# Optimization experiments

Measured on AMD Instinct MI355X. Metric: run time of the kernel, lower is better.

## Reference

```python
import jax, jax.numpy as jnp
import numpy as np

NJ, NS, NM, NR = 100000, 20000, 10000, 5000
D_IN, OUT, H = 128, 256, 4
C = OUT // H
E = 250000
NEG_SLOPE = 0.2
LN_EPS = 1e-5


def setup_inputs() -> dict:
    key = jax.random.key(0)
    ks = jax.random.split(key, 24)
    inp = {
        'x_job':     jax.random.normal(ks[0], (NJ, D_IN), jnp.float32),
        'x_station': jax.random.normal(ks[1], (NS, D_IN), jnp.float32),
        'x_machine': jax.random.normal(ks[2], (NM, D_IN), jnp.float32),
        'x_robot':   jax.random.normal(ks[3], (NR, D_IN), jnp.float32),
        'src_cl': jax.random.randint(ks[4],  (E,), 0, NS, jnp.int32),
        'dst_cl': jax.random.randint(ks[5],  (E,), 0, NJ, jnp.int32),
        'src_ld': jax.random.randint(ks[6],  (E,), 0, NS, jnp.int32),
        'dst_ld': jax.random.randint(ks[7],  (E,), 0, NJ, jnp.int32),
        'src_we': jax.random.randint(ks[8],  (E,), 0, NM, jnp.int32),
        'dst_we': jax.random.randint(ks[9],  (E,), 0, NJ, jnp.int32),
        'src_ex': jax.random.randint(ks[10], (E,), 0, NM, jnp.int32),
        'dst_ex': jax.random.randint(ks[11], (E,), 0, NJ, jnp.int32),
        'src_hd': jax.random.randint(ks[12], (E,), 0, NR, jnp.int32),
        'dst_hd': jax.random.randint(ks[13], (E,), 0, NJ, jnp.int32),
        'Ws':      jax.random.normal(ks[14], (5, D_IN, OUT), jnp.float32) * 0.05,
        'att_src': jax.random.normal(ks[15], (5, H, C), jnp.float32) * 0.05,
        'att_dst': jax.random.normal(ks[16], (5, H, C), jnp.float32) * 0.05,
        'biases':  jnp.zeros((5, OUT), jnp.float32),
        'W_res':   jax.random.normal(ks[17], (D_IN, OUT), jnp.float32) * 0.05,
        'ln_gamma': jnp.ones((OUT,), jnp.float32),
        'ln_beta':  jnp.zeros((OUT,), jnp.float32),
    }
    return inp


def _gat(x_src, x_dst, src, dst, W, a_src, a_dst, b):
    # Bipartite GATConv (PyG semantics, shared lin for src and dst, concat heads)
    hs = (x_src @ W).reshape(-1, H, C)   # [Ns,H,C]
    hd = (x_dst @ W).reshape(-1, H, C)   # [Nd,H,C]
    a_s = jnp.einsum('nhc,hc->nh', hs, a_src)  # [Ns,H]
    a_d = jnp.einsum('nhc,hc->nh', hd, a_dst)  # [Nd,H]
    e = jax.nn.leaky_relu(a_s[src] + a_d[dst], NEG_SLOPE)  # [E,H]
    # softmax over incoming edges of each dst node
    m = jax.ops.segment_max(e, dst, num_segments=NJ)       # [Nd,H]
    ex = jnp.exp(e - m[dst])
    denom = jax.ops.segment_sum(ex, dst, num_segments=NJ)
    alpha = ex / (denom[dst] + 1e-16)                       # [E,H]
    msg = alpha[:, :, None] * hs[src]                        # [E,H,C]
    out = jax.ops.segment_sum(msg, dst, num_segments=NJ)    # [Nd,H,C]
    return out.reshape(NJ, H * C) + b


def reference(x_job, x_station, x_machine, x_robot,
              src_cl, dst_cl, src_ld, dst_ld, src_we, dst_we,
              src_ex, dst_ex, src_hd, dst_hd,
              Ws, att_src, att_dst, biases, W_res, ln_gamma, ln_beta):
    rels = [
        (x_station, src_cl, dst_cl),
        (x_station, src_ld, dst_ld),
        (x_machine, src_we, dst_we),
        (x_machine, src_ex, dst_ex),
        (x_robot,   src_hd, dst_hd),
    ]
    acc = jnp.zeros((NJ, OUT), x_job.dtype)
    for i, (xs, s, d) in enumerate(rels):  # sum aggregation across relations
        acc = acc + _gat(xs, x_job, s, d, Ws[i], att_src[i], att_dst[i], biases[i])
    h = acc + x_job @ W_res                # residual projection (dj != out_dim)
    h = jax.nn.relu(h)
    mu = jnp.mean(h, axis=-1, keepdims=True)
    var = jnp.var(h, axis=-1, keepdims=True)
    return (h - mu) * jax.lax.rsqrt(var + LN_EPS) * ln_gamma + ln_beta
```

## Files before the change

### kernel.cpp

```cpp
#include <hip/hip_runtime.h>

typedef unsigned short u16;
typedef unsigned int u32;
typedef unsigned long long u64;
typedef __attribute__((ext_vector_type(8))) short s16x8;
typedef __attribute__((ext_vector_type(4))) float f32x4;

__device__ __forceinline__ float bf2f(u16 u) { return __uint_as_float(((u32)u) << 16); }
__device__ __forceinline__ u16 f2bf(float f) {
    u32 b = __float_as_uint(f);
    b += 0x7fffu + ((b >> 16) & 1u);
    return (u16)(b >> 16);
}

__global__ void probe_mark(float* __restrict__ out, int n, float val) {
    int i = blockIdx.x * blockDim.x + threadIdx.x;
    if (i < n) out[i] = val;
}

struct PrepX { const float* x[4]; int rows[4]; int blks[4]; u16* xb[4]; };

__global__ void k_prep_all(const float* __restrict__ Ws, const float* __restrict__ W_res,
                           const float* __restrict__ att_src, const float* __restrict__ att_dst,
                           const float* __restrict__ biases,
                           u32* __restrict__ cnt, int zc, int nzb, u16* __restrict__ wt,
                           float* __restrict__ w_d_all, float* __restrict__ w_s_cat,
                           float* __restrict__ bias_sum, PrepX PX) {
    int b = blockIdx.x;
    if (b < nzb) {
        int i = b * 256 + threadIdx.x;
        if (i < zc) cnt[i] = 0u;
        return;
    }
    b -= nzb;
    if (b < 768) {
        int i = b * 256 + threadIdx.x;
        int k = i & 127;
        int c = (i >> 7) & 255;
        int w = i >> 15;
        float v = (w < 5) ? Ws[(size_t)w * 32768 + k * 256 + c] : W_res[k * 256 + c];
        wt[i] = f2bf(v);
        return;
    }
    b -= 768;
    if (b < 6) {
        if (b < 5) {
            int k = threadIdx.x;
            if (k >= 128) return;
            const float* Wr = Ws + (size_t)b * 128 * 256 + (size_t)k * 256;
            for (int h = 0; h < 4; ++h) {
                float ss = 0.f, sd = 0.f;
                for (int c = 0; c < 64; ++c) {
                    float w = Wr[h * 64 + c];
                    ss += w * att_src[(b * 4 + h) * 64 + c];
                    sd += w * att_dst[(b * 4 + h) * 64 + c];
                }
                w_d_all[k * 20 + b * 4 + h] = sd;
                w_s_cat[b * 512 + k * 4 + h] = ss;
            }
        } else if (threadIdx.x < 256) {
            float s = 0.f;
            for (int r = 0; r < 5; ++r) s += biases[r * 256 + threadIdx.x];
            bias_sum[threadIdx.x] = s;
        }
        return;
    }
    b -= 6;
#pragma unroll
    for (int a = 0; a < 4; ++a) {
        if (b < PX.blks[a]) {
            int elem = b * 2048 + threadIdx.x * 8;
            if (elem < PX.rows[a] * 128) {
                const float4* src = (const float4*)(PX.x[a] + elem);
                float4 v0 = src[0], v1 = src[1];
                u32 w0 = ((u32)f2bf(v0.y) << 16) | f2bf(v0.x);
                u32 w1 = ((u32)f2bf(v0.w) << 16) | f2bf(v0.z);
                u32 w2 = ((u32)f2bf(v1.y) << 16) | f2bf(v1.x);
                u32 w3 = ((u32)f2bf(v1.w) << 16) | f2bf(v1.z);
                *(uint4*)(PX.xb[a] + elem) = make_uint4(w0, w1, w2, w3);
            }
            return;
        }
        b -= PX.blks[a];
    }
}

struct SDesc { const float* A; const float* W; float* out; int N; int Kout; int groups; int start; };
struct STab { SDesc d[6]; int total; };
struct GDesc { const u16* A; u16* C; int wslice; int N; int start; };
struct GTab { GDesc d[6]; };
struct EdgeP { const int* src[5]; const int* dst[5]; int base[5]; };

__global__ __launch_bounds__(256) void k_mid(GTab T, const u16* __restrict__ wt,
                                             STab S, EdgeP P,
                                             u32* __restrict__ cnt, u32* __restrict__ epos,
                                             int E, int nEB, int G, int C, int SB) {
    __shared__ __align__(16) u16 sA[64][136];
    __shared__ __align__(16) u16 sB[64][136];
    int q = blockIdx.x / 11, p = blockIdx.x % 11;
    int t = threadIdx.x;

    if (p < 3) {
        int bx = q * 3 + p;
        if (bx >= G) return;
        int mi = 0;
#pragma unroll
        for (int i = 1; i < 6; ++i) if (bx >= T.d[i].start) mi = i;
        GDesc d = T.d[mi];
        int R0 = (bx - d.start) * 64;
        int r = t >> 2, seg = (t & 3) * 32;
        {
            uint4 a0, a1, a2, a3;
            if (R0 + r < d.N) {
                const uint4* pa = (const uint4*)(d.A + (size_t)(R0 + r) * 128 + seg);
                a0 = pa[0]; a1 = pa[1]; a2 = pa[2]; a3 = pa[3];
            } else {
                a0 = a1 = a2 = a3 = make_uint4(0, 0, 0, 0);
            }
            uint4* qd = (uint4*)&sA[r][seg];
            qd[0] = a0; qd[1] = a1; qd[2] = a2; qd[3] = a3;
        }
        int wave = t >> 6, lane = t & 63;
        int quad = lane >> 4, m = lane & 15;
        const u16* aRow = &sA[wave * 16 + m][0];
        const u16* wbase = wt + (size_t)d.wslice * 32768;

        for (int y = 0; y < 4; ++y) {
            int c0 = y * 64;
            const uint4* pb = (const uint4*)(wbase + (size_t)(c0 + r) * 128 + seg);
            uint4 b0 = pb[0], b1 = pb[1], b2 = pb[2], b3 = pb[3];
            __syncthreads();
            uint4* qb = (uint4*)&sB[r][seg];
            qb[0] = b0; qb[1] = b1; qb[2] = b2; qb[3] = b3;
            __syncthreads();

            f32x4 acc[4] = {};
#pragma unroll
            for (int k0 = 0; k0 < 128; k0 += 32) {
                s16x8 af = *(const s16x8*)(aRow + k0 + quad * 8);
#pragma unroll
                for (int ct = 0; ct < 4; ++ct) {
                    s16x8 bf = *(const s16x8*)(&sB[ct * 16 + m][k0 + quad * 8]);
                    acc[ct] = __builtin_amdgcn_mfma_f32_16x16x32_bf16(af, bf, acc[ct], 0, 0, 0);
                }
            }
#pragma unroll
            for (int ct = 0; ct < 4; ++ct) {
#pragma unroll
                for (int i = 0; i < 4; ++i) {
                    int row = R0 + wave * 16 + quad * 4 + i;
                    if (row < d.N) d.C[(size_t)row * 256 + c0 + ct * 16 + m] = f2bf(acc[ct][i]);
                }
            }
        }
    } else if (p < 8) {
        int i = q * 5 + (p - 3);
        if (i >= C) return;
        int r = i / nEB, eb = i - r * nEB;
        int e = eb * 256 + t;
        if (e >= E) return;
        u32 c = atomicAdd(cnt + (size_t)P.dst[r][e] * 5 + r, 1u);
        epos[(size_t)r * E + e] = c;
    } else {
        int i = q * 3 + (p - 8);
        if (i >= SB) return;
        int idx = i * 256 + t;
        if (idx >= S.total) return;
        int mi = 0;
#pragma unroll
        for (int j = 1; j < 6; ++j) if (idx >= S.d[j].start) mi = j;
        SDesc d = S.d[mi];
        int local = idx - d.start;
        int row = local / d.groups, g = local - row * d.groups;
        const float* a = d.A + (size_t)row * 128;
        const float* w = d.W + g * 4;
        int Kout = d.Kout;
        float s0 = 0.f, s1 = 0.f, s2 = 0.f, s3 = 0.f;
        for (int k = 0; k < 128; k += 4) {
            float4 av = *(const float4*)(a + k);
            float4 w0 = *(const float4*)(w + (size_t)(k + 0) * Kout);
            float4 w1 = *(const float4*)(w + (size_t)(k + 1) * Kout);
            float4 w2 = *(const float4*)(w + (size_t)(k + 2) * Kout);
            float4 w3 = *(const float4*)(w + (size_t)(k + 3) * Kout);
            s0 += av.x * w0.x + av.y * w1.x + av.z * w2.x + av.w * w3.x;
            s1 += av.x * w0.y + av.y * w1.y + av.z * w2.y + av.w * w3.y;
            s2 += av.x * w0.z + av.y * w1.z + av.z * w2.z + av.w * w3.z;
            s3 += av.x * w0.w + av.y * w1.w + av.z * w2.w + av.w * w3.w;
        }
        float* o = d.out + (size_t)row * Kout + g * 4;
        *(float4*)o = make_float4(s0, s1, s2, s3);
    }
}

__global__ void k_scan1(const u32* __restrict__ cnt, u32* __restrict__ off,
                        u32* __restrict__ bsum, int nblk) {
    int b = blockIdx.x, t = threadIdx.x;
    size_t base = (size_t)b * 1024 + t * 4;
    u32 v0 = cnt[base], v1 = cnt[base + 1], v2 = cnt[base + 2], v3 = cnt[base + 3];
    u32 tsum = v0 + v1 + v2 + v3;
    __shared__ u32 s[256];
    u32 x = tsum;
    s[t] = x; __syncthreads();
    for (int ofs = 1; ofs < 256; ofs <<= 1) {
        u32 y = (t >= ofs) ? s[t - ofs] : 0u;
        __syncthreads();
        x += y; s[t] = x;
        __syncthreads();
    }
    u32 ex = x - tsum;
    off[base] = ex; off[base + 1] = ex + v0; off[base + 2] = ex + v0 + v1; off[base + 3] = ex + v0 + v1 + v2;
    if (t == 255) bsum[b] = x;
}

__global__ void k_scan23(u32* __restrict__ off, const u32* __restrict__ bsum, int nblk) {
    int b = blockIdx.x, t = threadIdx.x;
    __shared__ u32 s[256];
    u32 part = 0;
    for (int i = t; i < b; i += 256) part += bsum[i];
    s[t] = part; __syncthreads();
    for (int ofs = 128; ofs; ofs >>= 1) {
        if (t < ofs) s[t] += s[t + ofs];
        __syncthreads();
    }
    u32 add = s[0];
    size_t base = (size_t)b * 1024 + t * 4;
    off[base] += add; off[base + 1] += add; off[base + 2] += add; off[base + 3] += add;
}

__global__ void k_fill(EdgeP P, const u32* __restrict__ off, const u32* __restrict__ epos,
                       u32* __restrict__ epay, int E) {
    int r = blockIdx.y;
    int e = blockIdx.x * blockDim.x + threadIdx.x;
    if (e >= E) return;
    int d = P.dst[r][e];
    u32 pos = off[(size_t)d * 5 + r] + epos[(size_t)r * E + e];
    epay[pos] = (u32)(P.base[r] + P.src[r][e]);
}

__global__ __launch_bounds__(512) void k_gather(
        const u32* __restrict__ offs, const u32* __restrict__ epay,
        const float* __restrict__ as_h,
        const float* __restrict__ a_d,
        const u16* __restrict__ hs, const u16* __restrict__ resb,
        const float* __restrict__ bias_sum,
        const float* __restrict__ gamma, const float* __restrict__ beta,
        float* __restrict__ out, int NJ) {
    int row = blockIdx.x * 8 + (threadIdx.x >> 6);
    int lane = threadIdx.x & 63;
    if (row >= NJ) return;

    ushort4 rr = *(const ushort4*)(resb + (size_t)row * 256 + lane * 4);
    float4 bb = *(const float4*)(bias_sum + lane * 4);
    int c = lane * 4;
    float4 g = *(const float4*)(gamma + c);
    float4 be = *(const float4*)(beta + c);

    int hd = lane >> 4;
    u32 hoff = (u32)(lane << 2);

    const float* adb = a_d + (size_t)row * 20 + hd;
    float adx[5] = { adb[0], adb[4], adb[8], adb[12], adb[16] };

    const u32* op = offs + (size_t)row * 5;
    u32 o[6];
#pragma unroll
    for (int i = 0; i < 6; ++i) o[i] = op[i];
    u32 deg = o[5] - o[0];

    u32 pv = 0;
    if (deg) {
        u32 li = (u32)lane < deg ? (u32)lane : 0u;
        pv = epay[o[0] + li];
    }

    float a0 = 0.f, a1 = 0.f, a2 = 0.f, a3 = 0.f;
#pragma unroll
    for (int r = 0; r < 5; ++r) {
        float adr = adx[r];
        float n0 = 0.f, n1 = 0.f, n2 = 0.f, n3 = 0.f, dsum = 0.f;
        for (u32 e = o[r]; e < o[r + 1]; ++e) {
            u32 i = e - o[0];
            u32 p;
            if (i < 64u) p = __shfl(pv, (int)i);
            else         p = epay[e];
            float x = as_h[p * 4 + (u32)hd] + adr;
            x = x > 0.f ? x : 0.2f * x;
            float w = __expf(x);
            dsum += w;
            ushort4 hv = *(const ushort4*)(hs + ((size_t)p << 8) + hoff);
            n0 += w * bf2f(hv.x); n1 += w * bf2f(hv.y);
            n2 += w * bf2f(hv.z); n3 += w * bf2f(hv.w);
        }
        float iv = 1.f / (dsum + 1e-16f);
        a0 += n0 * iv; a1 += n1 * iv; a2 += n2 * iv; a3 += n3 * iv;
    }

    float h0 = fmaxf(a0 + bf2f(rr.x) + bb.x, 0.f);
    float h1 = fmaxf(a1 + bf2f(rr.y) + bb.y, 0.f);
    float h2 = fmaxf(a2 + bf2f(rr.z) + bb.z, 0.f);
    float h3 = fmaxf(a3 + bf2f(rr.w) + bb.w, 0.f);
    float s = h0 + h1 + h2 + h3;
    float s2 = h0 * h0 + h1 * h1 + h2 * h2 + h3 * h3;
    for (int o2 = 32; o2; o2 >>= 1) {
        s += __shfl_xor(s, o2);
        s2 += __shfl_xor(s2, o2);
    }
    float mu = s * (1.f / 256.f);
    float var = s2 * (1.f / 256.f) - mu * mu;
    float rs = rsqrtf(var + 1e-5f);
    float4 o4;
    o4.x = (h0 - mu) * rs * g.x + be.x;
    o4.y = (h1 - mu) * rs * g.y + be.y;
    o4.z = (h2 - mu) * rs * g.z + be.z;
    o4.w = (h3 - mu) * rs * g.w + be.w;
    *(float4*)(out + (size_t)row * 256 + c) = o4;
}

static size_t align256(size_t x) { return (x + 255) & ~(size_t)255; }

extern "C" void kernel_launch(void* const* d_in, const int* in_sizes, int n_in,
                              void* d_out, int out_size, void* d_ws, size_t ws_size,
                              hipStream_t stream) {
    float* out = (float*)d_out;

    int NJ = in_sizes[0] / 128, NS = in_sizes[1] / 128, NM = in_sizes[2] / 128, NR = in_sizes[3] / 128;
    int E = in_sizes[4];
    bool cfg_ok = (n_in >= 21) && (out_size == NJ * 256)
        && (in_sizes[14] == 5 * 128 * 256) && (in_sizes[18] == 128 * 256)
        && (in_sizes[19] == 256) && (in_sizes[20] == 256);
    if (!cfg_ok) { probe_mark<<<8, 256, 0, stream>>>(out, 2048, 1000000.0f); return; }

    const float* x_job = (const float*)d_in[0];
    const float* x_st  = (const float*)d_in[1];
    const float* x_ma  = (const float*)d_in[2];
    const float* x_ro  = (const float*)d_in[3];
    EdgeP EP;
    EP.src[0] = (const int*)d_in[4];  EP.dst[0] = (const int*)d_in[5];
    EP.src[1] = (const int*)d_in[6];  EP.dst[1] = (const int*)d_in[7];
    EP.src[2] = (const int*)d_in[8];  EP.dst[2] = (const int*)d_in[9];
    EP.src[3] = (const int*)d_in[10]; EP.dst[3] = (const int*)d_in[11];
    EP.src[4] = (const int*)d_in[12]; EP.dst[4] = (const int*)d_in[13];
    EP.base[0] = 0; EP.base[1] = NS; EP.base[2] = 2 * NS;
    EP.base[3] = 2 * NS + NM; EP.base[4] = 2 * NS + 2 * NM;
    const float* Ws      = (const float*)d_in[14];
    const float* att_src = (const float*)d_in[15];
    const float* att_dst = (const float*)d_in[16];
    const float* biases  = (const float*)d_in[17];
    const float* W_res   = (const float*)d_in[18];
    const float* gamma   = (const float*)d_in[19];
    const float* beta    = (const float*)d_in[20];

    int nseg = 5 * NJ;
    int nblk = (nseg + 1023) / 1024;
    int NPAD = nblk * 1024;
    int TOT = 2 * NS + 2 * NM + NR;
    int TOTX = NJ + NS + NM + NR;

    char* base = (char*)d_ws;
    size_t ob = 0;
    float*  w_d_all  = (float*)(base + ob);  ob += align256(128 * 20 * 4);
    float*  w_s_cat  = (float*)(base + ob);  ob += align256(5 * 128 * 4 * 4);
    float*  bias_sum = (float*)(base + ob);  ob += align256(256 * 4);
    float*  a_d      = (float*)(base + ob);  ob += align256((size_t)NJ * 20 * 4);
    float*  as_cat   = (float*)(base + ob);  ob += align256((size_t)TOT * 4 * 4);
    u16*    wt       = (u16*)(base + ob);    ob += align256((size_t)6 * 256 * 128 * 2);
    u16*    xb       = (u16*)(base + ob);    ob += align256((size_t)TOTX * 128 * 2);
    u16*    resb     = (u16*)(base + ob);    ob += align256((size_t)NJ * 256 * 2);
    u16*    hs_cat   = (u16*)(base + ob);    ob += align256((size_t)TOT * 256 * 2);
    u32*    cnt      = (u32*)(base + ob);    ob += align256((size_t)NPAD * 4);
    u32*    offs     = (u32*)(base + ob);    ob += align256((size_t)NPAD * 4);
    u32*    bsum     = (u32*)(base + ob);    ob += align256((size_t)nblk * 4);
    u32*    epos     = (u32*)(base + ob);    ob += align256((size_t)5 * E * 4);
    u32*    epay     = (u32*)(base + ob);    ob += align256((size_t)5 * E * 4);

    if (ws_size < ob) { probe_mark<<<8, 256, 0, stream>>>(out, 2048, 500000.0f); return; }

    int zc = NPAD;
    int nzb = (zc + 255) / 256;
    PrepX PX;
    PX.x[0] = x_job; PX.x[1] = x_st; PX.x[2] = x_ma; PX.x[3] = x_ro;
    PX.rows[0] = NJ; PX.rows[1] = NS; PX.rows[2] = NM; PX.rows[3] = NR;
    u16* xb_job = xb;
    u16* xb_st  = xb + (size_t)NJ * 128;
    u16* xb_ma  = xb + (size_t)(NJ + NS) * 128;
    u16* xb_ro  = xb + (size_t)(NJ + NS + NM) * 128;
    PX.xb[0] = xb_job; PX.xb[1] = xb_st; PX.xb[2] = xb_ma; PX.xb[3] = xb_ro;
    int nxb = 0;
    for (int a = 0; a < 4; ++a) { PX.blks[a] = (PX.rows[a] * 128 + 2047) / 2048; nxb += PX.blks[a]; }
    k_prep_all<<<nzb + 768 + 6 + nxb, 256, 0, stream>>>(Ws, W_res, att_src, att_dst, biases,
                                                        cnt, zc, nzb, wt,
                                                        w_d_all, w_s_cat, bias_sum, PX);

    STab ST;
    int st = 0;
    ST.d[0] = {x_job, w_d_all,           a_d,                             NJ, 20, 5, st}; st += NJ * 5;
    ST.d[1] = {x_st,  w_s_cat + 0 * 512, as_cat + (size_t)EP.base[0] * 4, NS, 4, 1, st}; st += NS;
    ST.d[2] = {x_st,  w_s_cat + 1 * 512, as_cat + (size_t)EP.base[1] * 4, NS, 4, 1, st}; st += NS;
    ST.d[3] = {x_ma,  w_s_cat + 2 * 512, as_cat + (size_t)EP.base[2] * 4, NM, 4, 1, st}; st += NM;
    ST.d[4] = {x_ma,  w_s_cat + 3 * 512, as_cat + (size_t)EP.base[3] * 4, NM, 4, 1, st}; st += NM;
    ST.d[5] = {x_ro,  w_s_cat + 4 * 512, as_cat + (size_t)EP.base[4] * 4, NR, 4, 1, st}; st += NR;
    ST.total = st;

    int tJ = (NJ + 63) / 64, tS = (NS + 63) / 64, tM = (NM + 63) / 64, tR = (NR + 63) / 64;
    GTab GT;
    int gs = 0;
    GT.d[0] = {xb_job, resb,                              5, NJ, gs}; gs += tJ;
    GT.d[1] = {xb_st,  hs_cat + (size_t)EP.base[0] * 256, 0, NS, gs}; gs += tS;
    GT.d[2] = {xb_st,  hs_cat + (size_t)EP.base[1] * 256, 1, NS, gs}; gs += tS;
    GT.d[3] = {xb_ma,  hs_cat + (size_t)EP.base[2] * 256, 2, NM, gs}; gs += tM;
    GT.d[4] = {xb_ma,  hs_cat + (size_t)EP.base[3] * 256, 3, NM, gs}; gs += tM;
    GT.d[5] = {xb_ro,  hs_cat + (size_t)EP.base[4] * 256, 4, NR, gs}; gs += tR;

    int nEB = (E + 255) / 256;
    int G = gs, C = 5 * nEB, SB = (ST.total + 255) / 256;
    int stripes = (G + 2) / 3;
    if ((C + 4) / 5 > stripes) stripes = (C + 4) / 5;
    if ((SB + 2) / 3 > stripes) stripes = (SB + 2) / 3;
    k_mid<<<stripes * 11, 256, 0, stream>>>(GT, wt, ST, EP, cnt, epos, E, nEB, G, C, SB);

    k_scan1<<<nblk, 256, 0, stream>>>(cnt, offs, bsum, nblk);
    k_scan23<<<nblk, 256, 0, stream>>>(offs, bsum, nblk);
    k_fill<<<dim3(nEB, 5), 256, 0, stream>>>(EP, offs, epos, epay, E);

    k_gather<<<(NJ + 7) / 8, 512, 0, stream>>>(offs, epay, as_cat,
                                               a_d, hs_cat, resb, bias_sum,
                                               gamma, beta, out, NJ);
}
```

Measured before the change: 490.0 us.

## Fuse scan and CSR fill into one persistent kernel with grid barriers

Merges the two-pass prefix scan and the edge fill into a single launch, using global atomic counters as software grid barriers between the block scan, the offset fix-up and the scatter phase. The sync counters live right after the count array and are zeroed by widening the existing zero-fill range. This removes two kernel launches and their inter-kernel gaps. In exchange the kernel depends on every block being resident at once (about 968 blocks), or the spin barriers can deadlock, and the fill now uses a grid-stride loop.

New measurement: 697.2 us. +42.3%, slower.

```diff
diff --git a/kernel.cpp b/kernel.cpp
--- a/kernel.cpp
+++ b/kernel.cpp
@@ -192,49 +192,69 @@
     }
 }
 
-__global__ void k_scan1(const u32* __restrict__ cnt, u32* __restrict__ off,
-                        u32* __restrict__ bsum, int nblk) {
-    int b = blockIdx.x, t = threadIdx.x;
-    size_t base = (size_t)b * 1024 + t * 4;
-    u32 v0 = cnt[base], v1 = cnt[base + 1], v2 = cnt[base + 2], v3 = cnt[base + 3];
-    u32 tsum = v0 + v1 + v2 + v3;
-    __shared__ u32 s[256];
-    u32 x = tsum;
-    s[t] = x; __syncthreads();
-    for (int ofs = 1; ofs < 256; ofs <<= 1) {
-        u32 y = (t >= ofs) ? s[t - ofs] : 0u;
-        __syncthreads();
-        x += y; s[t] = x;
-        __syncthreads();
-    }
-    u32 ex = x - tsum;
-    off[base] = ex; off[base + 1] = ex + v0; off[base + 2] = ex + v0 + v1; off[base + 3] = ex + v0 + v1 + v2;
-    if (t == 255) bsum[b] = x;
-}
-
-__global__ void k_scan23(u32* __restrict__ off, const u32* __restrict__ bsum, int nblk) {
+__global__ __launch_bounds__(256) void k_scanfill(
+        EdgeP P, const u32* __restrict__ cnt, u32* __restrict__ offs,
+        u32* __restrict__ bsum, u32* __restrict__ sync,
+        const u32* __restrict__ epos, u32* __restrict__ epay,
+        int nblk, int E, int F) {
     int b = blockIdx.x, t = threadIdx.x;
     __shared__ u32 s[256];
-    u32 part = 0;
-    for (int i = t; i < b; i += 256) part += bsum[i];
-    s[t] = part; __syncthreads();
-    for (int ofs = 128; ofs; ofs >>= 1) {
-        if (t < ofs) s[t] += s[t + ofs];
+    if (b < nblk) {
+        size_t base = (size_t)b * 1024 + t * 4;
+        u32 v0 = cnt[base], v1 = cnt[base + 1], v2 = cnt[base + 2], v3 = cnt[base + 3];
+        u32 tsum = v0 + v1 + v2 + v3;
+        u32 x = tsum;
+        s[t] = x; __syncthreads();
+        for (int ofs = 1; ofs < 256; ofs <<= 1) {
+            u32 y = (t >= ofs) ? s[t - ofs] : 0u;
+            __syncthreads();
+            x += y; s[t] = x;
+            __syncthreads();
+        }
+        u32 ex = x - tsum;
+        u32 l0 = ex, l1 = ex + v0, l2 = ex + v0 + v1, l3 = ex + v0 + v1 + v2;
+        if (t == 255) {
+            bsum[b] = x;
+            __threadfence();
+            atomicAdd(&sync[0], 1u);
+        }
+        if (t == 0) { while (atomicAdd(&sync[0], 0u) < (u32)nblk) {} }
         __syncthreads();
-    }
-    u32 add = s[0];
-    size_t base = (size_t)b * 1024 + t * 4;
-    off[base] += add; off[base + 1] += add; off[base + 2] += add; off[base + 3] += add;
-}
-
-__global__ void k_fill(EdgeP P, const u32* __restrict__ off, const u32* __restrict__ epos,
-                       u32* __restrict__ epay, int E) {
-    int r = blockIdx.y;
-    int e = blockIdx.x * blockDim.x + threadIdx.x;
-    if (e >= E) return;
-    int d = P.dst[r][e];
-    u32 pos = off[(size_t)d * 5 + r] + epos[(size_t)r * E + e];
-    epay[pos] = (u32)(P.base[r] + P.src[r][e]);
+        __threadfence();
+        u32 part = 0;
+        for (int i = t; i < b; i += 256) part += bsum[i];
+        s[t] = part; __syncthreads();
+        for (int o2 = 128; o2; o2 >>= 1) {
+            if (t < o2) s[t] += s[t + o2];
+            __syncthreads();
+        }
+        u32 add = s[0];
+        offs[base] = l0 + add; offs[base + 1] = l1 + add;
+        offs[base + 2] = l2 + add; offs[base + 3] = l3 + add;
+        __threadfence();
+        __syncthreads();
+        if (t == 0) atomicAdd(&sync[1], 1u);
+        if (t == 0) { while (atomicAdd(&sync[1], 0u) < (u32)nblk) {} }
+        __syncthreads();
+        __threadfence();
+    } else {
+        if (t == 0) { while (atomicAdd(&sync[1], 0u) < (u32)nblk) {} }
+        __syncthreads();
+        __threadfence();
+    }
+    int gt = b * 256 + t, stride = F * 256;
+#pragma unroll
+    for (int r = 0; r < 5; ++r) {
+        const int* ds = P.dst[r];
+        const int* ss = P.src[r];
+        const u32* ep = epos + (size_t)r * E;
+        int baseR = P.base[r];
+        for (int e = gt; e < E; e += stride) {
+            int d = ds[e];
+            u32 pos = offs[(size_t)d * 5 + r] + ep[e];
+            epay[pos] = (u32)(baseR + ss[e]);
+        }
+    }
 }
 
 __global__ __launch_bounds__(512) void k_gather(
@@ -368,6 +388,7 @@
     u16*    resb     = (u16*)(base + ob);    ob += align256((size_t)NJ * 256 * 2);
     u16*    hs_cat   = (u16*)(base + ob);    ob += align256((size_t)TOT * 256 * 2);
     u32*    cnt      = (u32*)(base + ob);    ob += align256((size_t)NPAD * 4);
+    u32*    sync     = (u32*)(base + ob);    ob += align256(64 * 4);
     u32*    offs     = (u32*)(base + ob);    ob += align256((size_t)NPAD * 4);
     u32*    bsum     = (u32*)(base + ob);    ob += align256((size_t)nblk * 4);
     u32*    epos     = (u32*)(base + ob);    ob += align256((size_t)5 * E * 4);
@@ -375,7 +396,7 @@
 
     if (ws_size < ob) { probe_mark<<<8, 256, 0, stream>>>(out, 2048, 500000.0f); return; }
 
-    int zc = NPAD;
+    int zc = NPAD + 64;
     int nzb = (zc + 255) / 256;
     PrepX PX;
     PX.x[0] = x_job; PX.x[1] = x_st; PX.x[2] = x_ma; PX.x[3] = x_ro;
@@ -418,9 +439,8 @@
     if ((SB + 2) / 3 > stripes) stripes = (SB + 2) / 3;
     k_mid<<<stripes * 11, 256, 0, stream>>>(GT, wt, ST, EP, cnt, epos, E, nEB, G, C, SB);
 
-    k_scan1<<<nblk, 256, 0, stream>>>(cnt, offs, bsum, nblk);
-    k_scan23<<<nblk, 256, 0, stream>>>(offs, bsum, nblk);
-    k_fill<<<dim3(nEB, 5), 256, 0, stream>>>(EP, offs, epos, epay, E);
+    int F = nblk > 968 ? nblk : 968;
+    k_scanfill<<<F, 256, 0, stream>>>(EP, cnt, offs, bsum, sync, epos, epay, nblk, E, F);
 
     k_gather<<<(NJ + 7) / 8, 512, 0, stream>>>(offs, epay, as_cat,
                                                a_d, hs_cat, resb, bias_sum,
```
